# Kernel tuning notes

Hardware: AMD Instinct MI355X
Metric: run time of the kernel (lower is better)

The kernel has to match this reference:

```python
import jax, jax.numpy as jnp
import numpy as np

B = 512          # graphs
M = 200          # nodes per graph
N = B * M        # 102400 total nodes
E = N * 32       # 3,276,800 edges
DIM_IN = 128
K = 30           # SortPool k
F = 32 + 32 + 32 + 1  # concat feature dim = 97


def setup_inputs() -> dict:
    key = jax.random.key(0)
    ks = jax.random.split(key, 20)
    x = jax.random.normal(ks[0], (N, DIM_IN), jnp.float32)
    # within-graph random edges so that batched SortPool is meaningful
    eg = jnp.repeat(jnp.arange(B, dtype=jnp.int32), E // B)  # graph id per edge
    src = eg * M + jax.random.randint(ks[1], (E,), 0, M, dtype=jnp.int32)
    dst = eg * M + jax.random.randint(ks[2], (E,), 0, M, dtype=jnp.int32)
    edge_index = jnp.stack([src, dst])  # [2, E]
    batch = jnp.arange(N, dtype=jnp.int32) // M  # sorted graph assignment

    def lin(k, fi, fo):
        s = 1.0 / np.sqrt(fi)
        return jax.random.uniform(k, (fi, fo), jnp.float32, -s, s)

    inp = {
        "x": x, "edge_index": edge_index, "batch": batch,
        "W1": lin(ks[3], DIM_IN, 32), "b1": jnp.zeros((32,), jnp.float32),
        "W2": lin(ks[4], 32, 32), "b2": jnp.zeros((32,), jnp.float32),
        "W3": lin(ks[5], 32, 32), "b3": jnp.zeros((32,), jnp.float32),
        "W4": lin(ks[6], 32, 1),  "b4": jnp.zeros((1,), jnp.float32),
        "convW1": jax.random.normal(ks[7], (16, 1, 97), jnp.float32) * 0.05,
        "convb1": jnp.zeros((16,), jnp.float32),
        "convW2": jax.random.normal(ks[8], (32, 16, 5), jnp.float32) * 0.05,
        "convb2": jnp.zeros((32,), jnp.float32),
        "linW1": lin(ks[9], 352, 128), "linb1": jnp.zeros((128,), jnp.float32),
        "linW2": lin(ks[10], 128, 1),  "linb2": jnp.zeros((1,), jnp.float32),
    }
    return inp


def _gcn(x, W, b, src, dst, dinv):
    """PyG GCNConv: D^-1/2 (A+I) D^-1/2 X W + b (degrees include self-loops)."""
    xw = x @ W                                   # [N, Fout]
    norm = dinv[src] * dinv[dst]                 # [E]
    agg = jax.ops.segment_sum(xw[src] * norm[:, None], dst, num_segments=N)
    agg = agg + xw * (dinv * dinv)[:, None]      # self-loop term
    return agg + b


def reference(x, edge_index, batch, W1, b1, W2, b2, W3, b3, W4, b4,
              convW1, convb1, convW2, convb2, linW1, linb1, linW2, linb2):
    src, dst = edge_index[0], edge_index[1]
    deg = jax.ops.segment_sum(jnp.ones((E,), x.dtype), dst, num_segments=N) + 1.0
    dinv = jax.lax.rsqrt(deg)

    h1 = jnp.tanh(_gcn(x, W1, b1, src, dst, dinv))
    h2 = jnp.tanh(_gcn(h1, W2, b2, src, dst, dinv))
    h3 = jnp.tanh(_gcn(h2, W3, b3, src, dst, dinv))
    h4 = jnp.tanh(_gcn(h3, W4, b4, src, dst, dinv))
    h = jnp.concatenate([h1, h2, h3, h4], axis=-1)  # [N, 97]

    # SortPool: batch is block-contiguous with M nodes/graph -> dense [B, M, F]
    hd = h.reshape(B, M, F)
    order = jnp.argsort(-hd[:, :, -1], axis=1)[:, :K]          # top-K by last channel
    top = jnp.take_along_axis(hd, order[:, :, None], axis=1)   # [B, K, 97]

    seq = top.reshape(B, 1, K * F)                             # [B, 1, 2910]
    dn = ("NCH", "OIH", "NCH")
    c1 = jax.lax.conv_general_dilated(seq, convW1, (97,), "VALID",
                                      dimension_numbers=dn) + convb1[None, :, None]
    c1 = jax.nn.relu(c1)                                       # [B, 16, 30]
    c1 = c1.reshape(B, 16, 15, 2).max(axis=-1)                 # MaxPool1d(2,2)
    c2 = jax.lax.conv_general_dilated(c1, convW2, (1,), "VALID",
                                      dimension_numbers=dn) + convb2[None, :, None]
    c2 = jax.nn.relu(c2)                                       # [B, 32, 11]

    flat = c2.reshape(B, 352)
    hlin = jax.nn.relu(flat @ linW1 + linb1)                   # dropout = identity (eval)
    out = jax.nn.sigmoid(hlin @ linW2 + linb2)                 # [B, 1]
    return out
```

## Files before the change

kernel.cpp:

```cpp
#include <hip/hip_runtime.h>
#include <hip/hip_fp16.h>


#define TPB   512
#define GRID  512
#define MG    200
#define EPG   6400
#define EE    (512 * EPG)

#define OFF_BUFX 0
#define OFF_HCUR 28944
#define OFF_CSR  57744
#define OFF_ROFF 64944
#define OFF_CNT  65760
#define OFF_CUR  66560
#define OFF_DINV 67360
#define OFF_H4   68160
#define OFF_RANK 68960
#define OFF_ORD  69760
#define OFF_BIAS 69880
#define OFF_RED  70136
#define OFF_WREG 70208
#define SMEM_BYTES 74560

#define QPAD 0xC8C8C8C8u

__device__ __forceinline__ float fast_tanh(float x) {
    const float e = __expf(2.0f * x);
    return 1.0f - 2.0f / (e + 1.0f);
}

__global__ __launch_bounds__(TPB)
void dgcnn_kernel(
    const float* __restrict__ x,
    const int*   __restrict__ ei,
    const float* __restrict__ W1, const float* __restrict__ b1,
    const float* __restrict__ W2, const float* __restrict__ b2,
    const float* __restrict__ W3, const float* __restrict__ b3,
    const float* __restrict__ W4, const float* __restrict__ b4,
    const float* __restrict__ cW1, const float* __restrict__ cb1,
    const float* __restrict__ cW2, const float* __restrict__ cb2,
    const float* __restrict__ lW1, const float* __restrict__ lb1,
    const float* __restrict__ lW2, const float* __restrict__ lb2,
    __half* __restrict__ arch,
    float* __restrict__ out)
{
    extern __shared__ unsigned char smem[];
    float* bufX = (float*)(smem + OFF_BUFX);
    float* hcur = (float*)(smem + OFF_HCUR);
    unsigned char* csr = (unsigned char*)(smem + OFF_CSR);
    int*   roff = (int*)(smem + OFF_ROFF);
    int*   cnt  = (int*)(smem + OFF_CNT);
    int*   cur  = (int*)(smem + OFF_CUR);
    float* dinv = (float*)(smem + OFF_DINV);
    float* h4k  = (float*)(smem + OFF_H4);
    int*   rank = (int*)(smem + OFF_RANK);
    int*   ord  = (int*)(smem + OFF_ORD);
    float* bias = (float*)(smem + OFF_BIAS);
    float* red  = (float*)(smem + OFF_RED);
    float* wreg = (float*)(smem + OFF_WREG);

    const int g = blockIdx.x;
    const int t = threadIdx.x;
    const int gbase = g * MG;
    const float* xg   = x + (size_t)gbase * 128;
    const int*   srcp = ei + (size_t)g * EPG;
    const int*   dstp = ei + (size_t)EE + (size_t)g * EPG;

    for (int idx = t; idx < 4096; idx += TPB)
        hcur[(idx & 31) * 132 + (idx >> 5)] = W1[idx];
    if (t < 32) bias[t] = b1[t];
    if (t < MG) { cnt[t] = 0; rank[t] = 0; }
    if (t >= 256 && t < 292) bufX[200 * 36 + (t - 256)] = 0.f;
    __syncthreads();

    const int f32lane = t & 31;
    const int islot   = t >> 5;

    {
        const int4* d4p = (const int4*)dstp;
        for (int e4 = t; e4 < EPG / 4; e4 += TPB) {
            const int4 d4 = d4p[e4];
            atomicAdd(&cnt[d4.x - gbase], 1);
            atomicAdd(&cnt[d4.y - gbase], 1);
            atomicAdd(&cnt[d4.z - gbase], 1);
            atomicAdd(&cnt[d4.w - gbase], 1);
        }
    }
    {
        const int f = f32lane;
        const float* wt = hcur + f * 132;
        const float4* xv = (const float4*)xg;
        #pragma unroll
        for (int j0 = 0; j0 < 12; j0 += 6) {
            const int r0 = islot + 16 * j0;
            float a0 = 0.f, a1 = 0.f, a2 = 0.f, a3 = 0.f, a4 = 0.f, a5 = 0.f;
            #pragma unroll 2
            for (int k4 = 0; k4 < 32; ++k4) {
                const float4 w = *(const float4*)(wt + 4 * k4);
                float4 v;
                v = xv[(r0      ) * 32 + k4]; a0 += v.x*w.x + v.y*w.y + v.z*w.z + v.w*w.w;
                v = xv[(r0 + 16 ) * 32 + k4]; a1 += v.x*w.x + v.y*w.y + v.z*w.z + v.w*w.w;
                v = xv[(r0 + 32 ) * 32 + k4]; a2 += v.x*w.x + v.y*w.y + v.z*w.z + v.w*w.w;
                v = xv[(r0 + 48 ) * 32 + k4]; a3 += v.x*w.x + v.y*w.y + v.z*w.z + v.w*w.w;
                v = xv[(r0 + 64 ) * 32 + k4]; a4 += v.x*w.x + v.y*w.y + v.z*w.z + v.w*w.w;
                v = xv[(r0 + 80 ) * 32 + k4]; a5 += v.x*w.x + v.y*w.y + v.z*w.z + v.w*w.w;
            }
            bufX[(r0      ) * 36 + f] = a0;
            bufX[(r0 + 16 ) * 36 + f] = a1;
            bufX[(r0 + 32 ) * 36 + f] = a2;
            bufX[(r0 + 48 ) * 36 + f] = a3;
            bufX[(r0 + 64 ) * 36 + f] = a4;
            bufX[(r0 + 80 ) * 36 + f] = a5;
        }
        if (islot < 8) {
            const int r = 192 + islot;
            float a0 = 0.f;
            #pragma unroll 2
            for (int k4 = 0; k4 < 32; ++k4) {
                const float4 w = *(const float4*)(wt + 4 * k4);
                const float4 v = xv[r * 32 + k4];
                a0 += v.x*w.x + v.y*w.y + v.z*w.z + v.w*w.w;
            }
            bufX[r * 36 + f] = a0;
        }
    }
    __syncthreads();

    if (t >= 256 && t < 256 + MG) {
        int i = t - 256;
        dinv[i] = 1.0f / sqrtf((float)(cnt[i] + 1));
    }
    if (t < 64) {
        if (t == 0) roff[0] = 0;
        int carry = 0;
        #pragma unroll
        for (int c = 0; c < 4; ++c) {
            const int i = c * 64 + t;
            int v = (i < MG) ? ((cnt[i] + 4) & ~3) : 0;
            #pragma unroll
            for (int off = 1; off < 64; off <<= 1) {
                int u = __shfl_up(v, off);
                if (t >= (int)off) v += u;
            }
            if (i < MG) roff[i + 1] = carry + v;
            carry += __shfl(v, 63);
        }
    }
    __syncthreads();

    if (t < MG) {
        int p = roff[t];
        csr[p] = (unsigned char)t;
        cur[t] = p + 1;
    }
    for (int r = islot; r < MG; r += 16) {
        bufX[r * 36 + f32lane] *= dinv[r];
    }
    __syncthreads();

    {
        const int4* s4p = (const int4*)srcp;
        const int4* d4p = (const int4*)dstp;
        for (int e4 = t; e4 < EPG / 4; e4 += TPB) {
            const int4 s4 = s4p[e4];
            const int4 d4 = d4p[e4];
            int p;
            p = atomicAdd(&cur[d4.x - gbase], 1); csr[p] = (unsigned char)(s4.x - gbase);
            p = atomicAdd(&cur[d4.y - gbase], 1); csr[p] = (unsigned char)(s4.y - gbase);
            p = atomicAdd(&cur[d4.z - gbase], 1); csr[p] = (unsigned char)(s4.z - gbase);
            p = atomicAdd(&cur[d4.w - gbase], 1); csr[p] = (unsigned char)(s4.w - gbase);
        }
    }
    __syncthreads();

    if (t < MG) {
        for (int p = cur[t]; p < roff[t + 1]; ++p) csr[p] = (unsigned char)200;
    }
    __syncthreads();

    auto agg_layer = [&](int archOff, int bb) {
        const int f4  = (t & 7) << 2;
        const int dsl = t >> 3;

        auto finish = [&](int d, float a0, float a1, float a2, float a3) {
            const float dv = dinv[d];
            const float o0 = fast_tanh(dv * a0 + bias[bb + f4 + 0]);
            const float o1 = fast_tanh(dv * a1 + bias[bb + f4 + 1]);
            const float o2 = fast_tanh(dv * a2 + bias[bb + f4 + 2]);
            const float o3 = fast_tanh(dv * a3 + bias[bb + f4 + 3]);
            *(float4*)(hcur + d * 36 + f4) = make_float4(o0, o1, o2, o3);
            if (archOff >= 0) {
                const __half2 p01 = __floats2half2_rn(o0, o1);
                const __half2 p23 = __floats2half2_rn(o2, o3);
                __half2* dst = (__half2*)(arch + (size_t)(gbase + d) * 64 + archOff + f4);
                dst[0] = p01;
                dst[1] = p23;
            }
        };

        auto pair_rows = [&](int da, int db) {
            const int p1a = roff[da + 1], p1b = roff[db + 1];
            int pa = roff[da], pb = roff[db];
            const int na = (p1a - pa) >> 2, nb = (p1b - pb) >> 2;
            const int iters = na > nb ? na : nb;
            unsigned qa = *(const unsigned*)(csr + pa);
            unsigned qb = *(const unsigned*)(csr + pb);
            float a0=0.f,a1=0.f,a2=0.f,a3=0.f, c0=0.f,c1=0.f,c2=0.f,c3=0.f;
            for (int i = 0; i < iters; ++i) {
                pa += 4; pb += 4;
                const unsigned qa_n = (pa < p1a) ? *(const unsigned*)(csr + pa) : QPAD;
                const unsigned qb_n = (pb < p1b) ? *(const unsigned*)(csr + pb) : QPAD;
                float4 v;
                v = *(const float4*)(bufX + (qa & 255u) * 36 + f4);         a0+=v.x; a1+=v.y; a2+=v.z; a3+=v.w;
                v = *(const float4*)(bufX + ((qa >> 8) & 255u) * 36 + f4);  a0+=v.x; a1+=v.y; a2+=v.z; a3+=v.w;
                v = *(const float4*)(bufX + ((qa >> 16) & 255u) * 36 + f4); a0+=v.x; a1+=v.y; a2+=v.z; a3+=v.w;
                v = *(const float4*)(bufX + (qa >> 24) * 36 + f4);          a0+=v.x; a1+=v.y; a2+=v.z; a3+=v.w;
                v = *(const float4*)(bufX + (qb & 255u) * 36 + f4);         c0+=v.x; c1+=v.y; c2+=v.z; c3+=v.w;
                v = *(const float4*)(bufX + ((qb >> 8) & 255u) * 36 + f4);  c0+=v.x; c1+=v.y; c2+=v.z; c3+=v.w;
                v = *(const float4*)(bufX + ((qb >> 16) & 255u) * 36 + f4); c0+=v.x; c1+=v.y; c2+=v.z; c3+=v.w;
                v = *(const float4*)(bufX + (qb >> 24) * 36 + f4);          c0+=v.x; c1+=v.y; c2+=v.z; c3+=v.w;
                qa = qa_n; qb = qb_n;
            }
            finish(da, a0, a1, a2, a3);
            finish(db, c0, c1, c2, c3);
        };

        auto one_row = [&](int d) {
            const int p1 = roff[d + 1];
            int p = roff[d];
            const int iters = (p1 - p) >> 2;
            unsigned q = *(const unsigned*)(csr + p);
            float a0=0.f,a1=0.f,a2=0.f,a3=0.f;
            for (int i = 0; i < iters; ++i) {
                p += 4;
                const unsigned q_n = (p < p1) ? *(const unsigned*)(csr + p) : QPAD;
                float4 v;
                v = *(const float4*)(bufX + (q & 255u) * 36 + f4);         a0+=v.x; a1+=v.y; a2+=v.z; a3+=v.w;
                v = *(const float4*)(bufX + ((q >> 8) & 255u) * 36 + f4);  a0+=v.x; a1+=v.y; a2+=v.z; a3+=v.w;
                v = *(const float4*)(bufX + ((q >> 16) & 255u) * 36 + f4); a0+=v.x; a1+=v.y; a2+=v.z; a3+=v.w;
                v = *(const float4*)(bufX + (q >> 24) * 36 + f4);          a0+=v.x; a1+=v.y; a2+=v.z; a3+=v.w;
                q = q_n;
            }
            finish(d, a0, a1, a2, a3);
        };

        pair_rows(dsl, dsl + 64);
        if (dsl < 8) pair_rows(dsl + 128, dsl + 192);
        else         one_row(dsl + 128);
    };

    auto gemm_mid = [&](const float* __restrict__ src) {
        const int f2 = t & 15;
        const int sl = t >> 4;
        const float* wp = wreg + f2 * 68;
        {
            float a0A=0.f,a1A=0.f,a2A=0.f,a3A=0.f,a4A=0.f,a5A=0.f;
            float a0B=0.f,a1B=0.f,a2B=0.f,a3B=0.f,a4B=0.f,a5B=0.f;
            #pragma unroll 2
            for (int k4 = 0; k4 < 8; ++k4) {
                const float4 wA = *(const float4*)(wp + k4 * 8);
                const float4 wB = *(const float4*)(wp + k4 * 8 + 4);
                float4 v;
                v = *(const float4*)(src + (sl       ) * 36 + 4 * k4);
                a0A += v.x*wA.x + v.y*wA.y + v.z*wA.z + v.w*wA.w;
                a0B += v.x*wB.x + v.y*wB.y + v.z*wB.z + v.w*wB.w;
                v = *(const float4*)(src + (sl + 32  ) * 36 + 4 * k4);
                a1A += v.x*wA.x + v.y*wA.y + v.z*wA.z + v.w*wA.w;
                a1B += v.x*wB.x + v.y*wB.y + v.z*wB.z + v.w*wB.w;
                v = *(const float4*)(src + (sl + 64  ) * 36 + 4 * k4);
                a2A += v.x*wA.x + v.y*wA.y + v.z*wA.z + v.w*wA.w;
                a2B += v.x*wB.x + v.y*wB.y + v.z*wB.z + v.w*wB.w;
                v = *(const float4*)(src + (sl + 96  ) * 36 + 4 * k4);
                a3A += v.x*wA.x + v.y*wA.y + v.z*wA.z + v.w*wA.w;
                a3B += v.x*wB.x + v.y*wB.y + v.z*wB.z + v.w*wB.w;
                v = *(const float4*)(src + (sl + 128 ) * 36 + 4 * k4);
                a4A += v.x*wA.x + v.y*wA.y + v.z*wA.z + v.w*wA.w;
                a4B += v.x*wB.x + v.y*wB.y + v.z*wB.z + v.w*wB.w;
                v = *(const float4*)(src + (sl + 160 ) * 36 + 4 * k4);
                a5A += v.x*wA.x + v.y*wA.y + v.z*wA.z + v.w*wA.w;
                a5B += v.x*wB.x + v.y*wB.y + v.z*wB.z + v.w*wB.w;
            }
            const int c0 = 2 * f2;
            *(float2*)(bufX + (sl       ) * 36 + c0) = make_float2(dinv[sl      ] * a0A, dinv[sl      ] * a0B);
            *(float2*)(bufX + (sl + 32  ) * 36 + c0) = make_float2(dinv[sl + 32 ] * a1A, dinv[sl + 32 ] * a1B);
            *(float2*)(bufX + (sl + 64  ) * 36 + c0) = make_float2(dinv[sl + 64 ] * a2A, dinv[sl + 64 ] * a2B);
            *(float2*)(bufX + (sl + 96  ) * 36 + c0) = make_float2(dinv[sl + 96 ] * a3A, dinv[sl + 96 ] * a3B);
            *(float2*)(bufX + (sl + 128 ) * 36 + c0) = make_float2(dinv[sl + 128] * a4A, dinv[sl + 128] * a4B);
            *(float2*)(bufX + (sl + 160 ) * 36 + c0) = make_float2(dinv[sl + 160] * a5A, dinv[sl + 160] * a5B);
        }
        if (sl < 8) {
            const int r = 192 + sl;
            float aA = 0.f, aB = 0.f;
            #pragma unroll 2
            for (int k4 = 0; k4 < 8; ++k4) {
                const float4 wA = *(const float4*)(wp + k4 * 8);
                const float4 wB = *(const float4*)(wp + k4 * 8 + 4);
                const float4 v = *(const float4*)(src + r * 36 + 4 * k4);
                aA += v.x*wA.x + v.y*wA.y + v.z*wA.z + v.w*wA.w;
                aB += v.x*wB.x + v.y*wB.y + v.z*wB.z + v.w*wB.w;
            }
            *(float2*)(bufX + r * 36 + 2 * f2) = make_float2(dinv[r] * aA, dinv[r] * aB);
        }
    };

    auto stage_w_paired = [&](const float* __restrict__ W) {
        for (int idx = t; idx < 1024; idx += TPB) {
            const int k = idx >> 5, f = idx & 31;
            wreg[(f >> 1) * 68 + (k >> 2) * 8 + ((f & 1) << 2) + (k & 3)] = W[idx];
        }
    };

    agg_layer(0, 0);
    stage_w_paired(W2);
    if (t < 32) bias[32 + t] = b2[t];
    __syncthreads();

    gemm_mid(hcur);
    __syncthreads();
    agg_layer(32, 32);
    stage_w_paired(W3);
    if (t < 32) bias[t] = b3[t];
    __syncthreads();

    gemm_mid(hcur);
    __syncthreads();
    agg_layer(-1, 0);
    __syncthreads();

    float* scl = (float*)(smem + OFF_CNT);
    if (t < MG) {
        float a = 0.f;
        #pragma unroll 8
        for (int k = 0; k < 32; ++k) a += hcur[t * 36 + k] * W4[k];
        scl[t] = dinv[t] * a;
    }
    if (t == 200) scl[200] = 0.f;
    __syncthreads();
    if (t < MG) {
        const int p0 = roff[t], p1 = roff[t + 1];
        float s = 0.f;
        for (int p = p0; p < p1; p += 4) {
            const unsigned q = *(const unsigned*)(csr + p);
            s += scl[q & 255u] + scl[(q >> 8) & 255u]
               + scl[(q >> 16) & 255u] + scl[q >> 24];
        }
        h4k[t] = fast_tanh(dinv[t] * s + b4[0]);
    }
    __syncthreads();

    {
        const int i = t & 255;
        const int half = t >> 8;
        if (i < MG) {
            const float vi = h4k[i];
            int r = 0;
            const int j0 = half * 100, j1 = half * 100 + 100;
            for (int j = j0; j < j1; ++j) {
                const float vj = h4k[j];
                r += (vj > vi || (vj == vi && j < i)) ? 1 : 0;
            }
            atomicAdd(&rank[i], r);
        }
    }
    __syncthreads();
    if (t < MG) {
        const int r = rank[t];
        if (r < 30) ord[r] = t;
    }
    __syncthreads();

    float* topv = bufX;
    float* cw   = bufX + 3104;
    for (int idx = t; idx < 1552; idx += TPB) cw[idx] = cW1[idx];
    for (int idx = t; idx < 2560; idx += TPB) cw[1552 + idx] = cW2[idx];
    if (t < 16) bias[t] = cb1[t];
    else if (t < 48) bias[t] = cb2[t - 16];
    for (int idx = t; idx < 2910; idx += TPB) {
        const int kk = idx / 97;
        const int ff = idx - kk * 97;
        const int nd = ord[kk];
        float v;
        if      (ff < 64) v = __half2float(arch[(size_t)(gbase + nd) * 64 + ff]);
        else if (ff < 96) v = hcur[nd * 36 + (ff - 64)];
        else              v = h4k[nd];
        topv[kk * 100 + ff] = v;
    }
    __syncthreads();

    float* c1p2 = hcur;
    float* c1pl = hcur + 480;
    float* flat = hcur + 736;
    float* hlin = hcur + 1088;

    if (t < 480) {
        const int o  = t & 15;
        const int tt = t >> 4;
        float a = bias[o];
        const float* wrow = cw + o * 97;
        const float* trow = topv + tt * 100;
        #pragma unroll 4
        for (int f = 0; f < 97; ++f) a += wrow[f] * trow[f];
        c1p2[o * 30 + tt] = fmaxf(a, 0.f);
    }
    __syncthreads();

    if (t < 240) {
        const int o  = t & 15;
        const int tp = t >> 4;
        c1pl[o * 16 + tp] = fmaxf(c1p2[o * 30 + 2 * tp], c1p2[o * 30 + 2 * tp + 1]);
    }
    __syncthreads();

    if (t < 352) {
        const int o  = t & 31;
        const int tt = t >> 5;
        float a = bias[16 + o];
        const float* w2r = cw + 1552 + o * 80;
        #pragma unroll
        for (int i2 = 0; i2 < 16; ++i2) {
            #pragma unroll
            for (int kk = 0; kk < 5; ++kk)
                a += w2r[i2 * 5 + kk] * c1pl[i2 * 16 + tt + kk];
        }
        flat[o * 11 + tt] = fmaxf(a, 0.f);
    } else if (t >= 352 && t < 480) {
        hlin[t - 352] = lb1[t - 352];
    }
    __syncthreads();

    {
        const int f  = t & 127;
        const int kc = t >> 7;
        float a = 0.f;
        const int k0 = kc * 88;
        #pragma unroll 4
        for (int kk = k0; kk < k0 + 88; ++kk) a += flat[kk] * lW1[kk * 128 + f];
        atomicAdd(&hlin[f], a);
    }
    __syncthreads();

    if (t < 128) {
        float p = fmaxf(hlin[t], 0.f) * lW2[t];
        #pragma unroll
        for (int off = 32; off > 0; off >>= 1) p += __shfl_down(p, off);
        if ((t & 63) == 0) red[t >> 6] = p;
    }
    __syncthreads();
    if (t == 0) {
        const float z = red[0] + red[1] + lb2[0];
        out[g] = 1.f / (1.f + expf(-z));
    }
}

extern "C" void kernel_launch(void* const* d_in, const int* in_sizes, int n_in,
                              void* d_out, int out_size, void* d_ws, size_t ws_size,
                              hipStream_t stream) {
    (void)in_sizes; (void)n_in; (void)out_size; (void)ws_size;
    const float* x   = (const float*)d_in[0];
    const int*   ei  = (const int*)d_in[1];
    const float* W1  = (const float*)d_in[3];  const float* b1  = (const float*)d_in[4];
    const float* W2  = (const float*)d_in[5];  const float* b2  = (const float*)d_in[6];
    const float* W3  = (const float*)d_in[7];  const float* b3  = (const float*)d_in[8];
    const float* W4  = (const float*)d_in[9];  const float* b4  = (const float*)d_in[10];
    const float* cW1 = (const float*)d_in[11]; const float* cb1 = (const float*)d_in[12];
    const float* cW2 = (const float*)d_in[13]; const float* cb2 = (const float*)d_in[14];
    const float* lW1 = (const float*)d_in[15]; const float* lb1 = (const float*)d_in[16];
    const float* lW2 = (const float*)d_in[17]; const float* lb2 = (const float*)d_in[18];
    float* out = (float*)d_out;
    __half* arch = (__half*)d_ws;

    hipFuncSetAttribute((const void*)dgcnn_kernel,
                        hipFuncAttributeMaxDynamicSharedMemorySize, SMEM_BYTES);

    dgcnn_kernel<<<GRID, TPB, SMEM_BYTES, stream>>>(
        x, ei, W1, b1, W2, b2, W3, b3, W4, b4,
        cW1, cb1, cW2, cb2, lW1, lb1, lW2, lb2, arch, out);
}
```

Baseline: 246.4 us.

## Sort aggregation rows by degree, prefill CSR padding, overlap conv weight staging

Each node's in-degree is bucketed into a histogram, then prefix-summed into a permutation that orders nodes by degree. Aggregation threads are assigned rows from this permutation so paired rows in a wavefront have similar trip counts, which reduces divergence. The CSR buffer is prefilled with the pad byte, removing the separate padding pass and one barrier. Conv weight loads are moved earlier to overlap with the h4 computation, and the cW2 rows are padded to stride 81 to avoid LDS bank conflicts. This costs extra shared memory and atomics for the histogram.

```diff
diff --git a/kernel.cpp b/kernel.cpp
--- a/kernel.cpp
+++ b/kernel.cpp
@@ -21,7 +21,9 @@
 #define OFF_BIAS 69880
 #define OFF_RED  70136
 #define OFF_WREG 70208
-#define SMEM_BYTES 74560
+#define OFF_HIST 74560
+#define OFF_PERM 74688
+#define SMEM_BYTES 75488
 
 #define QPAD 0xC8C8C8C8u
 
@@ -59,6 +61,8 @@
     float* bias = (float*)(smem + OFF_BIAS);
     float* red  = (float*)(smem + OFF_RED);
     float* wreg = (float*)(smem + OFF_WREG);
+    int*   hist = (int*)(smem + OFF_HIST);
+    int*   perm = (int*)(smem + OFF_PERM);
 
     const int g = blockIdx.x;
     const int t = threadIdx.x;
@@ -69,8 +73,11 @@
 
     for (int idx = t; idx < 4096; idx += TPB)
         hcur[(idx & 31) * 132 + (idx >> 5)] = W1[idx];
+    for (int idx = t; idx < 1800; idx += TPB)
+        ((unsigned*)csr)[idx] = QPAD;
     if (t < 32) bias[t] = b1[t];
     if (t < MG) { cnt[t] = 0; rank[t] = 0; }
+    if (t >= 480) hist[t - 480] = 0;
     if (t >= 256 && t < 292) bufX[200 * 36 + (t - 256)] = 0.f;
     __syncthreads();
 
@@ -128,8 +135,12 @@
     __syncthreads();
 
     if (t >= 256 && t < 256 + MG) {
-        int i = t - 256;
-        dinv[i] = 1.0f / sqrtf((float)(cnt[i] + 1));
+        const int i = t - 256;
+        const int c = cnt[i];
+        dinv[i] = 1.0f / sqrtf((float)(c + 1));
+        int qc = (c + 4) >> 2;
+        if (qc > 31) qc = 31;
+        atomicAdd(&hist[31 - qc], 1);
     }
     if (t < 64) {
         if (t == 0) roff[0] = 0;
@@ -154,8 +165,15 @@
         csr[p] = (unsigned char)t;
         cur[t] = p + 1;
     }
-    for (int r = islot; r < MG; r += 16) {
-        bufX[r * 36 + f32lane] *= dinv[r];
+    if (t < 32) {
+        const int own = hist[t];
+        int v = own;
+        #pragma unroll
+        for (int off = 1; off < 32; off <<= 1) {
+            int u = __shfl_up(v, off);
+            if (t >= off) v += u;
+        }
+        hist[t] = v - own;
     }
     __syncthreads();
 
@@ -172,10 +190,14 @@
             p = atomicAdd(&cur[d4.w - gbase], 1); csr[p] = (unsigned char)(s4.w - gbase);
         }
     }
-    __syncthreads();
-
+    for (int r = islot; r < MG; r += 16) {
+        bufX[r * 36 + f32lane] *= dinv[r];
+    }
     if (t < MG) {
-        for (int p = cur[t]; p < roff[t + 1]; ++p) csr[p] = (unsigned char)200;
+        int qc = (cnt[t] + 4) >> 2;
+        if (qc > 31) qc = 31;
+        const int pos = atomicAdd(&hist[31 - qc], 1);
+        perm[pos] = t;
     }
     __syncthreads();
 
@@ -245,9 +267,9 @@
             finish(d, a0, a1, a2, a3);
         };
 
-        pair_rows(dsl, dsl + 64);
-        if (dsl < 8) pair_rows(dsl + 128, dsl + 192);
-        else         one_row(dsl + 128);
+        pair_rows(perm[2 * dsl], perm[2 * dsl + 1]);
+        if (dsl < 8) pair_rows(perm[128 + dsl], perm[192 + dsl]);
+        else         one_row(perm[128 + dsl]);
     };
 
     auto gemm_mid = [&](const float* __restrict__ src) {
@@ -328,6 +350,9 @@
     agg_layer(-1, 0);
     __syncthreads();
 
+    float* topv = bufX;
+    float* cw   = bufX + 3008;
+
     float* scl = (float*)(smem + OFF_CNT);
     if (t < MG) {
         float a = 0.f;
@@ -336,6 +361,13 @@
         scl[t] = dinv[t] * a;
     }
     if (t == 200) scl[200] = 0.f;
+    if (t >= 256) {
+        for (int idx = t - 256; idx < 1552; idx += 256) cw[idx] = cW1[idx];
+    } else if (t >= 208 && t < 224) {
+        bias[t - 208] = cb1[t - 208];
+    } else if (t >= 224 && t < 256) {
+        bias[16 + (t - 224)] = cb2[t - 224];
+    }
     __syncthreads();
     if (t < MG) {
         const int p0 = roff[t], p1 = roff[t + 1];
@@ -346,6 +378,12 @@
                + scl[(q >> 16) & 255u] + scl[q >> 24];
         }
         h4k[t] = fast_tanh(dinv[t] * s + b4[0]);
+    }
+    if (t >= 256) {
+        for (int idx = t - 256; idx < 2560; idx += 256) {
+            const int o = idx / 80, r = idx - o * 80;
+            cw[1552 + o * 81 + r] = cW2[idx];
+        }
     }
     __syncthreads();
 
@@ -370,12 +408,6 @@
     }
     __syncthreads();
 
-    float* topv = bufX;
-    float* cw   = bufX + 3104;
-    for (int idx = t; idx < 1552; idx += TPB) cw[idx] = cW1[idx];
-    for (int idx = t; idx < 2560; idx += TPB) cw[1552 + idx] = cW2[idx];
-    if (t < 16) bias[t] = cb1[t];
-    else if (t < 48) bias[t] = cb2[t - 16];
     for (int idx = t; idx < 2910; idx += TPB) {
         const int kk = idx / 97;
         const int ff = idx - kk * 97;
@@ -416,7 +448,7 @@
         const int o  = t & 31;
         const int tt = t >> 5;
         float a = bias[16 + o];
-        const float* w2r = cw + 1552 + o * 80;
+        const float* w2r = cw + 1552 + o * 81;
         #pragma unroll
         for (int i2 = 0; i2 < 16; ++i2) {
             #pragma unroll
```

New measurement: 237.6 us. 1.04x faster.
